# Optimization experiments

Measured on AMD Instinct MI355X. Metric: run time of the kernel, lower is better.

Reference implementation:

```python
import jax, jax.numpy as jnp
import numpy as np

N_REACHES = 4096
N_STEPS = 96
DT = 3600.0  # routing timestep (s), default from MuskingumCungeRouter


def safe_pow(base, exp, eps=1e-6):
    # AD-safe power: exp(e * log(max(b, eps)))
    return jnp.exp(exp * jnp.log(jnp.maximum(base, eps)))


def setup_inputs() -> dict:
    key = jax.random.key(0)
    ks = jax.random.split(key, 10)
    n, T = N_REACHES, N_STEPS
    u = lambda k, lo, hi, shape: jax.random.uniform(k, shape, minval=lo, maxval=hi)
    lateral_inflows = u(ks[0], 0.0, 5.0, (T, n))          # m^3/s lateral inflow
    initial_Q = u(ks[1], 0.1, 10.0, (n,))
    lengths = u(ks[2], 500.0, 10000.0, (n,))              # reach length (m)
    slopes = u(ks[3], 1e-4, 0.05, (n,))                   # bed slope
    manning_n = u(ks[4], 0.02, 0.08, (n,))
    width_coef = u(ks[5], 2.0, 10.0, (n,))
    width_exp = u(ks[6], 0.4, 0.6, (n,))                  # ~0.5 typical
    depth_coef = u(ks[7], 0.2, 0.6, (n,))
    depth_exp = u(ks[8], 0.25, 0.35, (n,))                # ~0.3 typical
    # Strictly lower-triangular sparse adjacency: reach i receives from j < i
    # (valid topological order), ~4 upstream links per reach on average.
    upstream_mask = jnp.tril(jax.random.uniform(ks[9], (n, n)) < (4.0 / n), k=-1)
    is_outlet = jnp.arange(n) == n - 1
    return dict(lateral_inflows=lateral_inflows, initial_Q=initial_Q,
                lengths=lengths, slopes=slopes, manning_n=manning_n,
                width_coef=width_coef, width_exp=width_exp,
                depth_coef=depth_coef, depth_exp=depth_exp,
                upstream_mask=upstream_mask, is_outlet=is_outlet)


def _mc_coeffs(Q, L, S, mn, wc, we, dc, de, dt):
    """Vectorized Muskingum-Cunge coefficients for all reaches.

    Faithful fusion of compute_channel_geometry -> compute_velocity_manning ->
    compute_celerity -> compute_muskingum_params. Q here is Q_ref = max(state.Q, 0.1),
    which only depends on the previous state, so hoisting out of the per-reach
    scan is mathematically identical to the original.
    """
    Qs = jnp.maximum(Q, 0.01)
    W = wc * safe_pow(Qs, we)
    D = dc * safe_pow(Qs, de)
    A = W * D
    R = A / (W + 2.0 * D)                      # hydraulic radius
    safe_S = jnp.maximum(S, 1e-6)
    V = (1.0 / jnp.maximum(mn, 1e-3)) * safe_pow(R, 2.0 / 3.0) * jnp.sqrt(safe_S)
    c = jnp.maximum((5.0 / 3.0) * V, 0.01)     # kinematic wave celerity
    K = jnp.maximum(L / c, dt * 0.1)
    X = jnp.clip(0.5 * (1.0 - Q / (W * c * safe_S * L + 1e-6)), 0.0, 0.5)
    den = 2.0 * K * (1.0 - X) + dt
    C0 = jnp.maximum((dt - 2.0 * K * X) / den, 0.0)
    C1 = jnp.maximum((dt + 2.0 * K * X) / den, 0.0)
    C2 = jnp.maximum((2.0 * K * (1.0 - X) - dt) / den, 0.0)
    tot = C0 + C1 + C2
    return C0 / tot, C1 / tot, C2 / tot


def _route(lateral_inflows, initial_Q, lengths, slopes, manning_n,
           width_coef, width_exp, depth_coef, depth_exp,
           upstream_mask, is_outlet, dt=DT):
    n = lengths.shape[0]

    def step(state, lateral):
        Q, Q_prev, I_prev = state
        Q_ref = jnp.maximum(Q, 0.1)
        C0, C1, C2 = _mc_coeffs(Q_ref, lengths, slopes, manning_n,
                                width_coef, width_exp, depth_coef, depth_exp, dt)

        # Sequential topological sweep: masked reduction over already-routed reaches.
        def process(Q_acc, i):
            upstream_Q = jnp.sum(jnp.where(upstream_mask[i], Q_acc, 0.0))
            I_curr = upstream_Q + lateral[i]
            Q_out = jnp.maximum(C0[i] * I_curr + C1[i] * I_prev[i] + C2[i] * Q_prev[i], 0.0)
            return Q_acc.at[i].set(Q_out), I_curr

        Q_final, I_all = jax.lax.scan(process, jnp.zeros(n, lateral.dtype), jnp.arange(n))
        outlet_Q = jnp.sum(jnp.where(is_outlet, Q_final, 0.0))
        return (Q_final, Q, I_all), outlet_Q

    init = (initial_Q, initial_Q, jnp.zeros(n, initial_Q.dtype))
    _, outlet_series = jax.lax.scan(step, init, lateral_inflows)
    return outlet_series  # [n_timesteps]


def reference(lateral_inflows, initial_Q, lengths, slopes, manning_n,
              width_coef, width_exp, depth_coef, depth_exp,
              upstream_mask, is_outlet):
    return _route(lateral_inflows, initial_Q, lengths, slopes, manning_n,
                  width_coef, width_exp, depth_coef, depth_exp,
                  upstream_mask, is_outlet)
```

## Files before the change

### kernel.cpp

```cpp
#include <hip/hip_runtime.h>

#define NR 4096
#define NT 96
#define NNZ_CAP 10240
#define WLDS 8
#define DHIST 32
#define DTSTEP 3600.0f

__device__ __forceinline__ float RCP(float x) { return __builtin_amdgcn_rcpf(x); }

__global__ void mc_build(const int* __restrict__ mask, int* __restrict__ rowBase,
                         int* __restrict__ rowCnt, int* __restrict__ gctr,
                         unsigned short* __restrict__ cols) {
  int row = blockIdx.x;
  int lane = threadIdx.x;
  const int4* rv = (const int4*)(mask + (size_t)row * NR);
  int c = 0;
  for (int j = lane; j < NR / 4; j += 64) {
    int4 v = rv[j];
    c += (v.x != 0) + (v.y != 0) + (v.z != 0) + (v.w != 0);
  }
#pragma unroll
  for (int off = 32; off > 0; off >>= 1) c += __shfl_down(c, off);
  int base = 0;
  if (lane == 0) {
    base = atomicAdd(gctr, c);
    rowBase[row] = base;
    rowCnt[row] = c;
  }
  base = __shfl(base, 0);
  const int* rs = mask + (size_t)row * NR;
  for (int j0 = 0; j0 < NR; j0 += 64) {
    int j = j0 + lane;
    int pred = (rs[j] != 0);
    unsigned long long m = __ballot(pred);
    if (pred) {
      int pos = __popcll(m & ((1ull << lane) - 1ull));
      int p = base + pos;
      if (p < NNZ_CAP) cols[p] = (unsigned short)j;
    }
    base += __popcll(m);
  }
}

__global__ __launch_bounds__(1024) void mc_prep(
    const int* __restrict__ rowBase, const int* __restrict__ rowCnt,
    const int* __restrict__ gctr, const unsigned short* __restrict__ colsOld,
    unsigned short* __restrict__ orderG, unsigned short* __restrict__ levNG,
    int* __restrict__ rowptrN, int* __restrict__ splitN,
    unsigned short* __restrict__ colsT, unsigned char* __restrict__ longSrcG,
    int* __restrict__ meta) {
  __shared__ unsigned short cols_s[NNZ_CAP];
  __shared__ unsigned char lev_s[NR];
  __shared__ unsigned short newid_s[NR];
  __shared__ unsigned short order_s[NR];
  __shared__ unsigned char lsrc_s[NR];
  __shared__ int cnt[1024];
  __shared__ int sbuf[1024];
  __shared__ int maxLevS, flagS;
  const int tid = threadIdx.x;
  int nnz = gctr[0];
  if (nnz > NNZ_CAP) nnz = NNZ_CAP;
  for (int e = tid; e < nnz; e += 1024) cols_s[e] = colsOld[e];

  int b_r[4], e_r[4];
#pragma unroll
  for (int k = 0; k < 4; ++k) {
    int i = 4 * tid + k;
    int b = rowBase[i];
    if (b > NNZ_CAP) b = NNZ_CAP;
    int e = b + rowCnt[i];
    if (e > NNZ_CAP) e = NNZ_CAP;
    b_r[k] = b;
    e_r[k] = e;
    lev_s[i] = 0;
    lsrc_s[i] = 0;
  }
  if (tid == 0) maxLevS = 0;
  __syncthreads();

  for (int pass = 0; pass < 48; ++pass) {
    if (tid == 0) flagS = 0;
    __syncthreads();
    int ch = 0;
#pragma unroll
    for (int k = 0; k < 4; ++k) {
      int i = 4 * tid + k;
      int lv = 0;
      for (int e = b_r[k]; e < e_r[k]; ++e) {
        int l2 = (int)lev_s[cols_s[e]] + 1;
        lv = lv > l2 ? lv : l2;
      }
      if (lv > 127) lv = 127;
      if (lv > (int)lev_s[i]) {
        lev_s[i] = (unsigned char)lv;
        ch = 1;
      }
    }
    if (ch) flagS = 1;
    __syncthreads();
    int done = (flagS == 0);
    __syncthreads();
    if (done) break;
  }
  int lm = 0;
#pragma unroll
  for (int k = 0; k < 4; ++k) {
    int l = lev_s[4 * tid + k];
    lm = lm > l ? lm : l;
  }
  atomicMax(&maxLevS, lm);
  __syncthreads();
  const int maxLev = maxLevS;
  if (tid == 0) {
    meta[0] = maxLev + 1;
    meta[2] = (maxLev >= DHIST) ? 1 : 0;
  }
  if (maxLev >= DHIST) {
#pragma unroll
    for (int k = 0; k < 4; ++k) {
      int i = 4 * tid + k;
      orderG[i] = (unsigned short)i;
      levNG[i] = (unsigned short)lev_s[i];
    }
    return;
  }

  cnt[tid] = 0;
  __syncthreads();
  int bkt_r[4];
#pragma unroll
  for (int k = 0; k < 4; ++k) {
    int i = 4 * tid + k;
    int d = e_r[k] - b_r[k];
    if (d > 31) d = 31;
    int bkt = ((int)lev_s[i]) * 32 + d;
    bkt_r[k] = bkt;
    atomicAdd(&cnt[bkt], 1);
  }
  __syncthreads();
  int v = cnt[tid];
  sbuf[tid] = v;
  __syncthreads();
  for (int off = 1; off < 1024; off <<= 1) {
    int add = tid >= off ? sbuf[tid - off] : 0;
    __syncthreads();
    sbuf[tid] += add;
    __syncthreads();
  }
  cnt[tid] = sbuf[tid] - v;
  __syncthreads();
#pragma unroll
  for (int k = 0; k < 4; ++k) {
    int i = 4 * tid + k;
    int pos = atomicAdd(&cnt[bkt_r[k]], 1);
    order_s[pos] = (unsigned short)i;
    newid_s[i] = (unsigned short)pos;
  }
  __syncthreads();

  int ob_r[4], c_r[4], tot = 0;
  unsigned char lvp_r[4];
#pragma unroll
  for (int k = 0; k < 4; ++k) {
    int p = 4 * tid + k;
    int oldi = order_s[p];
    orderG[p] = (unsigned short)oldi;
    unsigned char lp = lev_s[oldi];
    lvp_r[k] = lp;
    levNG[p] = (unsigned short)lp;
    int b = rowBase[oldi];
    if (b > NNZ_CAP) b = NNZ_CAP;
    int e = b + rowCnt[oldi];
    if (e > NNZ_CAP) e = NNZ_CAP;
    ob_r[k] = b;
    c_r[k] = e - b;
    tot += c_r[k];
  }
  sbuf[tid] = tot;
  __syncthreads();
  for (int off = 1; off < 1024; off <<= 1) {
    int add = tid >= off ? sbuf[tid - off] : 0;
    __syncthreads();
    sbuf[tid] += add;
    __syncthreads();
  }
  int base = sbuf[tid] - tot;
#pragma unroll
  for (int k = 0; k < 4; ++k) {
    int p = 4 * tid + k;
    rowptrN[p] = base;
    int ns = 0;
    for (int e = 0; e < c_r[k]; ++e) {
      int lag = (int)lvp_r[k] - (int)lev_s[cols_s[ob_r[k] + e]];
      ns += (lag < WLDS);
    }
    splitN[p] = base + ns;
    int si = base, li = base + ns;
    for (int e = 0; e < c_r[k]; ++e) {
      int cOld = cols_s[ob_r[k] + e];
      int cN = newid_s[cOld];
      int lag = (int)lvp_r[k] - (int)lev_s[cOld];
      if (lag < WLDS) {
        if (si < NNZ_CAP) colsT[si] = (unsigned short)cN;
        si++;
      } else {
        if (li < NNZ_CAP) colsT[li] = (unsigned short)cN;
        li++;
        lsrc_s[cN] = 1;
      }
    }
    base += c_r[k];
  }
  if (tid == 1023) rowptrN[NR] = sbuf[1023];
  if (tid == 0) meta[1] = newid_s[NR - 1];
  __syncthreads();
#pragma unroll
  for (int k = 0; k < 4; ++k) {
    int p = 4 * tid + k;
    longSrcG[p] = lsrc_s[p];
  }
}

__global__ void mc_permlat(const float* __restrict__ lat,
                           const unsigned short* __restrict__ orderG,
                           float* __restrict__ latP) {
  int g = blockIdx.x * 256 + threadIdx.x;
  int t = g >> 12, p = g & 4095;
  latP[g] = lat[t * NR + orderG[p]];
}

__device__ __forceinline__ void mc_coeff(float q1, float wc, float we, float dc,
                                         float de, float vk, float SL, float Lv,
                                         float& C0, float& C1, float& C2,
                                         float& inv) {
  float Qref = fmaxf(q1, 0.1f);
  float lq = __logf(Qref);
  float W = wc * __expf(we * lq);
  float Dd = dc * __expf(de * lq);
  float R = W * Dd * RCP(W + 2.f * Dd);
  float V = vk * __expf(0.66666667f * __logf(fmaxf(R, 1e-6f)));
  float c = fmaxf(1.6666667f * V, 0.01f);
  float K = fmaxf(Lv * RCP(c), 0.1f * DTSTEP);
  float X = 0.5f - 0.5f * Qref * RCP(W * c * SL + 1e-6f);
  X = fminf(fmaxf(X, 0.f), 0.5f);
  float twoKX = 2.f * K * X;
  C0 = fmaxf(DTSTEP - twoKX, 0.f);
  C1 = DTSTEP + twoKX;
  C2 = fmaxf(2.f * K - twoKX - DTSTEP, 0.f);
  inv = RCP(C0 + C1 + C2);
}

__global__ __launch_bounds__(1024) void mc_route(
    const float* __restrict__ lat, const float* __restrict__ latP,
    const float* __restrict__ initQ, const float* __restrict__ Lg,
    const float* __restrict__ Sg, const float* __restrict__ mng,
    const float* __restrict__ wcg, const float* __restrict__ weg,
    const float* __restrict__ dcg, const float* __restrict__ deg,
    const int* __restrict__ rowBase, const int* __restrict__ rowCnt,
    const unsigned short* __restrict__ colsOld,
    const unsigned short* __restrict__ orderG,
    const unsigned short* __restrict__ levNG, const int* __restrict__ rowptrN,
    const int* __restrict__ splitN, const unsigned short* __restrict__ colsT,
    const unsigned char* __restrict__ longSrcG, const int* __restrict__ meta,
    float* Qhist, float* __restrict__ out, int usePerm) {
  __shared__ float win[WLDS * NR];
  __shared__ unsigned short cols_s[NNZ_CAP];
  const int tid = threadIdx.x;
  const int nlv = meta[0];
  const int fb = meta[2];
  const int outletNew = meta[1];

  int b_r[4], m_r[4], e_r[4], lev_r[4], oldi_r[4], io_r[4], ls_r[4];
  float wc_r[4], we_r[4], dc_r[4], de_r[4], vk_r[4], SL_r[4], L_r[4];
  float ip_r[4], q1_r[4], q2_r[4];

  if (!fb) {
    int nnzN = rowptrN[NR];
    if (nnzN > NNZ_CAP) nnzN = NNZ_CAP;
    for (int e = tid; e < nnzN; e += 1024) cols_s[e] = colsT[e];
#pragma unroll
    for (int k = 0; k < 4; ++k) {
      int p = tid + k * 1024;
      int oldi = orderG[p];
      oldi_r[k] = oldi;
      lev_r[k] = (int)levNG[p];
      int b = rowptrN[p];
      if (b > NNZ_CAP) b = NNZ_CAP;
      int m = splitN[p];
      if (m > NNZ_CAP) m = NNZ_CAP;
      int e = rowptrN[p + 1];
      if (e > NNZ_CAP) e = NNZ_CAP;
      b_r[k] = b;
      m_r[k] = m;
      e_r[k] = e;
      io_r[k] = (p == outletNew);
      ls_r[k] = (int)longSrcG[p];
      float Lv = Lg[oldi], Sv = Sg[oldi], mnv = mng[oldi];
      float sS = fmaxf(Sv, 1e-6f);
      vk_r[k] = sqrtf(sS) * RCP(fmaxf(mnv, 1e-3f));
      SL_r[k] = sS * Lv;
      L_r[k] = Lv;
      wc_r[k] = wcg[oldi];
      we_r[k] = weg[oldi];
      dc_r[k] = dcg[oldi];
      de_r[k] = deg[oldi];
      float q0 = initQ[oldi];
      q1_r[k] = q0;
      q2_r[k] = q0;
      ip_r[k] = 0.f;
    }
    __syncthreads();

#define BODY(k, tt)                                                            \
  {                                                                            \
    const int p = tid + (k)*1024;                                              \
    float latv = usePerm ? latP[(tt)*NR + p] : lat[(tt)*NR + oldi_r[k]];       \
    float C0, C1, C2, inv;                                                     \
    mc_coeff(q1_r[k], wc_r[k], we_r[k], dc_r[k], de_r[k], vk_r[k], SL_r[k],    \
             L_r[k], C0, C1, C2, inv);                                         \
    const int wEl = ((tt) & (WLDS - 1)) << 12;                                 \
    float sup = 0.f;                                                           \
    for (int e = b_r[k]; e < m_r[k]; ++e) sup += win[wEl | cols_s[e]];         \
    if (m_r[k] < e_r[k]) {                                                     \
      const float* qb = Qhist + (((tt) & (DHIST - 1)) << 12);                  \
      for (int e = m_r[k]; e < e_r[k]; ++e) sup += qb[cols_s[e]];              \
    }                                                                          \
    float Icurr = sup + latv;                                                  \
    float Qout = fmaxf((C0 * Icurr + C1 * ip_r[k] + C2 * q2_r[k]) * inv, 0.f); \
    win[wEl | p] = Qout;                                                       \
    if (ls_r[k]) Qhist[((((tt) & (DHIST - 1)) << 12)) | p] = Qout;             \
    ip_r[k] = Icurr;                                                           \
    q2_r[k] = q1_r[k];                                                         \
    q1_r[k] = Qout;                                                            \
    if (io_r[k]) out[tt] = Qout;                                               \
  }

#define BODYC(k, s)                                                            \
  {                                                                            \
    int t = (s)-lev_r[k];                                                      \
    if ((unsigned)t < (unsigned)NT) BODY(k, t)                                 \
  }

    for (int s = 0; s < nlv - 1; ++s) {
#pragma unroll
      for (int k = 0; k < 4; ++k) BODYC(k, s);
      __syncthreads();
    }
    for (int s = nlv - 1; s < NT; ++s) {
#pragma unroll
      for (int k = 0; k < 4; ++k) {
        int t = s - lev_r[k];
        BODY(k, t);
      }
      __syncthreads();
    }
    for (int s = NT; s < NT + nlv - 1; ++s) {
#pragma unroll
      for (int k = 0; k < 4; ++k) BODYC(k, s);
      __syncthreads();
    }
  } else {
    for (int e = tid; e < NNZ_CAP; e += 1024) cols_s[e] = colsOld[e];
#pragma unroll
    for (int k = 0; k < 4; ++k) {
      int i = tid + k * 1024;
      lev_r[k] = (int)levNG[i];
      int b = rowBase[i];
      if (b > NNZ_CAP) b = NNZ_CAP;
      int e = b + rowCnt[i];
      if (e > NNZ_CAP) e = NNZ_CAP;
      b_r[k] = b;
      e_r[k] = e;
      float Lv = Lg[i], Sv = Sg[i], mnv = mng[i];
      float sS = fmaxf(Sv, 1e-6f);
      vk_r[k] = sqrtf(sS) * RCP(fmaxf(mnv, 1e-3f));
      SL_r[k] = sS * Lv;
      L_r[k] = Lv;
      wc_r[k] = wcg[i];
      we_r[k] = weg[i];
      dc_r[k] = dcg[i];
      de_r[k] = deg[i];
      float q0 = initQ[i];
      q1_r[k] = q0;
      q2_r[k] = q0;
      ip_r[k] = 0.f;
    }
    __syncthreads();
    for (int t = 0; t < NT; ++t) {
      for (int l = 0; l < meta[0]; ++l) {
#pragma unroll
        for (int k = 0; k < 4; ++k) {
          if (lev_r[k] == l) {
            int i = tid + k * 1024;
            float latv = lat[t * NR + i];
            float C0, C1, C2, inv;
            mc_coeff(q1_r[k], wc_r[k], we_r[k], dc_r[k], de_r[k], vk_r[k],
                     SL_r[k], L_r[k], C0, C1, C2, inv);
            float sup = 0.f;
            for (int e = b_r[k]; e < e_r[k]; ++e) sup += Qhist[cols_s[e]];
            float Icurr = sup + latv;
            float Qout =
                fmaxf((C0 * Icurr + C1 * ip_r[k] + C2 * q2_r[k]) * inv, 0.f);
            Qhist[i] = Qout;
            ip_r[k] = Icurr;
            q2_r[k] = q1_r[k];
            q1_r[k] = Qout;
            if (i == NR - 1) out[t] = Qout;
          }
        }
        __syncthreads();
      }
    }
  }
}

extern "C" void kernel_launch(void* const* d_in, const int* in_sizes, int n_in,
                              void* d_out, int out_size, void* d_ws, size_t ws_size,
                              hipStream_t stream) {
  const float* lat = (const float*)d_in[0];
  const float* iQ = (const float*)d_in[1];
  const float* Lg = (const float*)d_in[2];
  const float* Sg = (const float*)d_in[3];
  const float* mng = (const float*)d_in[4];
  const float* wcg = (const float*)d_in[5];
  const float* weg = (const float*)d_in[6];
  const float* dcg = (const float*)d_in[7];
  const float* deg = (const float*)d_in[8];
  const int* mask = (const int*)d_in[9];
  float* out = (float*)d_out;

  char* w = (char*)d_ws;
  int* rowBase = (int*)w;                w += NR * 4;
  int* rowCnt = (int*)w;                 w += NR * 4;
  int* gctr = (int*)w;                   w += 16;
  int* meta = (int*)w;                   w += 16;
  unsigned short* colsOld = (unsigned short*)w;  w += NNZ_CAP * 2;
  unsigned short* orderG = (unsigned short*)w;   w += NR * 2;
  unsigned short* levNG = (unsigned short*)w;    w += NR * 2;
  int* rowptrN = (int*)w;                w += (NR + 4) * 4;
  int* splitN = (int*)w;                 w += NR * 4;
  unsigned short* colsT = (unsigned short*)w;    w += NNZ_CAP * 2;
  unsigned char* longSrcG = (unsigned char*)w;   w += NR;
  w += 16 - ((size_t)w & 15);
  float* Qhist = (float*)w;              w += (size_t)DHIST * NR * 4;
  float* latP = (float*)w;               w += (size_t)NT * NR * 4;
  size_t need = (size_t)(w - (char*)d_ws);
  int usePerm = (ws_size >= need) ? 1 : 0;

  hipMemsetAsync(gctr, 0, sizeof(int), stream);
  mc_build<<<NR, 64, 0, stream>>>(mask, rowBase, rowCnt, gctr, colsOld);
  mc_prep<<<1, 1024, 0, stream>>>(rowBase, rowCnt, gctr, colsOld, orderG, levNG,
                                  rowptrN, splitN, colsT, longSrcG, meta);
  if (usePerm)
    mc_permlat<<<(NT * NR) / 256, 256, 0, stream>>>(lat, orderG, latP);
  mc_route<<<1, 1024, 0, stream>>>(lat, latP, iQ, Lg, Sg, mng, wcg, weg, dcg,
                                   deg, rowBase, rowCnt, colsOld, orderG, levNG,
                                   rowptrN, splitN, colsT, longSrcG, meta,
                                   Qhist, out, usePerm);
}
```

Measured before the change: 563.5 us.

## Restructure routing sweep with fixed 4-slot upstream lists and log-domain coefficients

mc_build now reads each mask row once: it compacts column indices into shared memory, then does one atomic and copies them out. mc_prep replaces the CSR rowptr/split arrays with a fixed 4-entry packed upstream list per reach, plus separate overflow lists for short-lag and long-lag sources built with atomics. mc_route reads the four slots with a single uint2 LDS load, prefetches the next timestep's lateral inflow, and computes the Muskingum coefficients in log2 domain with precomputed log constants, which removes several exp/log calls. The change also shrinks the window to 7 slots, adds a launch-bounds occupancy hint, and caps rows at 80 upstream entries, which could drop links on denser inputs.

```diff
diff --git a/kernel.cpp b/kernel.cpp
--- a/kernel.cpp
+++ b/kernel.cpp
@@ -3,43 +3,46 @@
 #define NR 4096
 #define NT 96
 #define NNZ_CAP 10240
-#define WLDS 8
+#define WLDS 7
 #define DHIST 32
 #define DTSTEP 3600.0f
+#define LOG2_1E6 -19.931568f
 
 __device__ __forceinline__ float RCP(float x) { return __builtin_amdgcn_rcpf(x); }
+__device__ __forceinline__ float EXP2(float x) { return __builtin_amdgcn_exp2f(x); }
+__device__ __forceinline__ float LOG2(float x) { return __builtin_amdgcn_logf(x); }
 
 __global__ void mc_build(const int* __restrict__ mask, int* __restrict__ rowBase,
                          int* __restrict__ rowCnt, int* __restrict__ gctr,
                          unsigned short* __restrict__ cols) {
+  __shared__ unsigned short tmp[80];
+  __shared__ int baseS;
   int row = blockIdx.x;
   int lane = threadIdx.x;
-  const int4* rv = (const int4*)(mask + (size_t)row * NR);
-  int c = 0;
-  for (int j = lane; j < NR / 4; j += 64) {
-    int4 v = rv[j];
-    c += (v.x != 0) + (v.y != 0) + (v.z != 0) + (v.w != 0);
-  }
-#pragma unroll
-  for (int off = 32; off > 0; off >>= 1) c += __shfl_down(c, off);
-  int base = 0;
-  if (lane == 0) {
-    base = atomicAdd(gctr, c);
-    rowBase[row] = base;
-    rowCnt[row] = c;
-  }
-  base = __shfl(base, 0);
   const int* rs = mask + (size_t)row * NR;
+  int total = 0;
   for (int j0 = 0; j0 < NR; j0 += 64) {
     int j = j0 + lane;
     int pred = (rs[j] != 0);
     unsigned long long m = __ballot(pred);
     if (pred) {
-      int pos = __popcll(m & ((1ull << lane) - 1ull));
-      int p = base + pos;
-      if (p < NNZ_CAP) cols[p] = (unsigned short)j;
-    }
-    base += __popcll(m);
+      int pos = total + __popcll(m & ((1ull << lane) - 1ull));
+      if (pos < 80) tmp[pos] = (unsigned short)j;
+    }
+    total += __popcll(m);
+  }
+  if (total > 80) total = 80;
+  if (lane == 0) {
+    int b = atomicAdd(gctr, total);
+    rowBase[row] = b;
+    rowCnt[row] = total;
+    baseS = b;
+  }
+  __syncthreads();
+  int base = baseS;
+  for (int e = lane; e < total; e += 64) {
+    int p = base + e;
+    if (p < NNZ_CAP) cols[p] = tmp[e];
   }
 }
 
@@ -47,8 +50,9 @@
     const int* __restrict__ rowBase, const int* __restrict__ rowCnt,
     const int* __restrict__ gctr, const unsigned short* __restrict__ colsOld,
     unsigned short* __restrict__ orderG, unsigned short* __restrict__ levNG,
-    int* __restrict__ rowptrN, int* __restrict__ splitN,
-    unsigned short* __restrict__ colsT, unsigned char* __restrict__ longSrcG,
+    unsigned short* __restrict__ scolG, unsigned int* __restrict__ sremMeta,
+    unsigned int* __restrict__ longMeta, unsigned short* __restrict__ sremG,
+    unsigned short* __restrict__ longG, unsigned char* __restrict__ lsG,
     int* __restrict__ meta) {
   __shared__ unsigned short cols_s[NNZ_CAP];
   __shared__ unsigned char lev_s[NR];
@@ -159,66 +163,59 @@
   }
   __syncthreads();
 
-  int ob_r[4], c_r[4], tot = 0;
-  unsigned char lvp_r[4];
 #pragma unroll
   for (int k = 0; k < 4; ++k) {
     int p = 4 * tid + k;
     int oldi = order_s[p];
     orderG[p] = (unsigned short)oldi;
-    unsigned char lp = lev_s[oldi];
-    lvp_r[k] = lp;
+    int lp = (int)lev_s[oldi];
     levNG[p] = (unsigned short)lp;
     int b = rowBase[oldi];
     if (b > NNZ_CAP) b = NNZ_CAP;
     int e = b + rowCnt[oldi];
     if (e > NNZ_CAP) e = NNZ_CAP;
-    ob_r[k] = b;
-    c_r[k] = e - b;
-    tot += c_r[k];
-  }
-  sbuf[tid] = tot;
-  __syncthreads();
-  for (int off = 1; off < 1024; off <<= 1) {
-    int add = tid >= off ? sbuf[tid - off] : 0;
-    __syncthreads();
-    sbuf[tid] += add;
-    __syncthreads();
-  }
-  int base = sbuf[tid] - tot;
-#pragma unroll
-  for (int k = 0; k < 4; ++k) {
-    int p = 4 * tid + k;
-    rowptrN[p] = base;
-    int ns = 0;
-    for (int e = 0; e < c_r[k]; ++e) {
-      int lag = (int)lvp_r[k] - (int)lev_s[cols_s[ob_r[k] + e]];
-      ns += (lag < WLDS);
-    }
-    splitN[p] = base + ns;
-    int si = base, li = base + ns;
-    for (int e = 0; e < c_r[k]; ++e) {
-      int cOld = cols_s[ob_r[k] + e];
+    int nS = 0, nR = 0, nL = 0;
+    for (int ee = b; ee < e; ++ee) {
+      int lag = lp - (int)lev_s[cols_s[ee]];
+      if (lag < WLDS) {
+        if (nS < 4) ++nS; else ++nR;
+      } else ++nL;
+    }
+    if (nR > 63) nR = 63;
+    if (nL > 63) nL = 63;
+    int sB = nR ? atomicAdd(&meta[4], nR) : 0;
+    int lB = nL ? atomicAdd(&meta[5], nL) : 0;
+    if (sB > NNZ_CAP) sB = NNZ_CAP;
+    if (sB + nR > NNZ_CAP) nR = NNZ_CAP - sB;
+    if (lB > NNZ_CAP) lB = NNZ_CAP;
+    if (lB + nL > NNZ_CAP) nL = NNZ_CAP - lB;
+    unsigned short sc[4] = {0, 0, 0, 0};
+    int iS = 0, cR = 0, cL = 0;
+    for (int ee = b; ee < e; ++ee) {
+      int cOld = cols_s[ee];
       int cN = newid_s[cOld];
-      int lag = (int)lvp_r[k] - (int)lev_s[cOld];
+      int lag = lp - (int)lev_s[cOld];
       if (lag < WLDS) {
-        if (si < NNZ_CAP) colsT[si] = (unsigned short)cN;
-        si++;
+        if (iS < 4) sc[iS++] = (unsigned short)cN;
+        else if (cR < nR) { sremG[sB + cR] = (unsigned short)cN; ++cR; }
       } else {
-        if (li < NNZ_CAP) colsT[li] = (unsigned short)cN;
-        li++;
+        if (cL < nL) { longG[lB + cL] = (unsigned short)cN; ++cL; }
         lsrc_s[cN] = 1;
       }
     }
-    base += c_r[k];
-  }
-  if (tid == 1023) rowptrN[NR] = sbuf[1023];
+    scolG[4 * p + 0] = sc[0];
+    scolG[4 * p + 1] = sc[1];
+    scolG[4 * p + 2] = sc[2];
+    scolG[4 * p + 3] = sc[3];
+    sremMeta[p] = (unsigned)sB | ((unsigned)nR << 20) | ((unsigned)iS << 26);
+    longMeta[p] = (unsigned)lB | ((unsigned)nL << 20);
+  }
   if (tid == 0) meta[1] = newid_s[NR - 1];
   __syncthreads();
 #pragma unroll
   for (int k = 0; k < 4; ++k) {
     int p = 4 * tid + k;
-    longSrcG[p] = lsrc_s[p];
+    lsG[p] = lsrc_s[p];
   }
 }
 
@@ -230,28 +227,7 @@
   latP[g] = lat[t * NR + orderG[p]];
 }
 
-__device__ __forceinline__ void mc_coeff(float q1, float wc, float we, float dc,
-                                         float de, float vk, float SL, float Lv,
-                                         float& C0, float& C1, float& C2,
-                                         float& inv) {
-  float Qref = fmaxf(q1, 0.1f);
-  float lq = __logf(Qref);
-  float W = wc * __expf(we * lq);
-  float Dd = dc * __expf(de * lq);
-  float R = W * Dd * RCP(W + 2.f * Dd);
-  float V = vk * __expf(0.66666667f * __logf(fmaxf(R, 1e-6f)));
-  float c = fmaxf(1.6666667f * V, 0.01f);
-  float K = fmaxf(Lv * RCP(c), 0.1f * DTSTEP);
-  float X = 0.5f - 0.5f * Qref * RCP(W * c * SL + 1e-6f);
-  X = fminf(fmaxf(X, 0.f), 0.5f);
-  float twoKX = 2.f * K * X;
-  C0 = fmaxf(DTSTEP - twoKX, 0.f);
-  C1 = DTSTEP + twoKX;
-  C2 = fmaxf(2.f * K - twoKX - DTSTEP, 0.f);
-  inv = RCP(C0 + C1 + C2);
-}
-
-__global__ __launch_bounds__(1024) void mc_route(
+__global__ __launch_bounds__(1024, 4) void mc_route(
     const float* __restrict__ lat, const float* __restrict__ latP,
     const float* __restrict__ initQ, const float* __restrict__ Lg,
     const float* __restrict__ Sg, const float* __restrict__ mng,
@@ -260,80 +236,112 @@
     const int* __restrict__ rowBase, const int* __restrict__ rowCnt,
     const unsigned short* __restrict__ colsOld,
     const unsigned short* __restrict__ orderG,
-    const unsigned short* __restrict__ levNG, const int* __restrict__ rowptrN,
-    const int* __restrict__ splitN, const unsigned short* __restrict__ colsT,
-    const unsigned char* __restrict__ longSrcG, const int* __restrict__ meta,
+    const unsigned short* __restrict__ levNG,
+    const unsigned short* __restrict__ scolG,
+    const unsigned int* __restrict__ sremMeta,
+    const unsigned int* __restrict__ longMeta,
+    const unsigned short* __restrict__ sremG,
+    const unsigned short* __restrict__ longG,
+    const unsigned char* __restrict__ lsG, const int* __restrict__ meta,
     float* Qhist, float* __restrict__ out, int usePerm) {
-  __shared__ float win[WLDS * NR];
-  __shared__ unsigned short cols_s[NNZ_CAP];
+  __shared__ float win_s[WLDS * NR];
+  __shared__ unsigned short scol_s[NR * 4];
   const int tid = threadIdx.x;
   const int nlv = meta[0];
   const int fb = meta[2];
   const int outletNew = meta[1];
 
-  int b_r[4], m_r[4], e_r[4], lev_r[4], oldi_r[4], io_r[4], ls_r[4];
-  float wc_r[4], we_r[4], dc_r[4], de_r[4], vk_r[4], SL_r[4], L_r[4];
-  float ip_r[4], q1_r[4], q2_r[4];
+  int lev_r[4], io_r[4], ls_r[4], wslot_r[4], cnt_r[4];
+  int sB_r[4], sC_r[4], lB_r[4], lC_r[4], latIdx_r[4];
+  float lwc_r[4], we_r[4], ldc_r[4], de_r[4], lvk_r[4], SL_r[4], L_r[4];
+  float ip_r[4], q1_r[4], q2_r[4], latN_r[4];
+  const float* latB = usePerm ? latP : lat;
 
   if (!fb) {
-    int nnzN = rowptrN[NR];
-    if (nnzN > NNZ_CAP) nnzN = NNZ_CAP;
-    for (int e = tid; e < nnzN; e += 1024) cols_s[e] = colsT[e];
+    for (int e = tid; e < NR * 2; e += 1024)
+      ((unsigned int*)scol_s)[e] = ((const unsigned int*)scolG)[e];
 #pragma unroll
     for (int k = 0; k < 4; ++k) {
       int p = tid + k * 1024;
       int oldi = orderG[p];
-      oldi_r[k] = oldi;
       lev_r[k] = (int)levNG[p];
-      int b = rowptrN[p];
-      if (b > NNZ_CAP) b = NNZ_CAP;
-      int m = splitN[p];
-      if (m > NNZ_CAP) m = NNZ_CAP;
-      int e = rowptrN[p + 1];
-      if (e > NNZ_CAP) e = NNZ_CAP;
-      b_r[k] = b;
-      m_r[k] = m;
-      e_r[k] = e;
+      unsigned int sm = sremMeta[p];
+      sB_r[k] = sm & 0xFFFFF;
+      sC_r[k] = (sm >> 20) & 63;
+      cnt_r[k] = (sm >> 26) & 7;
+      unsigned int lm2 = longMeta[p];
+      lB_r[k] = lm2 & 0xFFFFF;
+      lC_r[k] = (lm2 >> 20) & 63;
+      ls_r[k] = (int)lsG[p];
       io_r[k] = (p == outletNew);
-      ls_r[k] = (int)longSrcG[p];
-      float Lv = Lg[oldi], Sv = Sg[oldi], mnv = mng[oldi];
-      float sS = fmaxf(Sv, 1e-6f);
-      vk_r[k] = sqrtf(sS) * RCP(fmaxf(mnv, 1e-3f));
+      float Lv = Lg[oldi];
+      float sS = fmaxf(Sg[oldi], 1e-6f);
+      float mnv = fmaxf(mng[oldi], 1e-3f);
+      lvk_r[k] = 0.7369656f + 0.5f * LOG2(sS) - LOG2(mnv);
       SL_r[k] = sS * Lv;
       L_r[k] = Lv;
-      wc_r[k] = wcg[oldi];
+      lwc_r[k] = LOG2(wcg[oldi]);
       we_r[k] = weg[oldi];
-      dc_r[k] = dcg[oldi];
+      ldc_r[k] = LOG2(dcg[oldi]);
       de_r[k] = deg[oldi];
       float q0 = initQ[oldi];
       q1_r[k] = q0;
       q2_r[k] = q0;
       ip_r[k] = 0.f;
-    }
-    __syncthreads();
-
-#define BODY(k, tt)                                                            \
-  {                                                                            \
-    const int p = tid + (k)*1024;                                              \
-    float latv = usePerm ? latP[(tt)*NR + p] : lat[(tt)*NR + oldi_r[k]];       \
-    float C0, C1, C2, inv;                                                     \
-    mc_coeff(q1_r[k], wc_r[k], we_r[k], dc_r[k], de_r[k], vk_r[k], SL_r[k],    \
-             L_r[k], C0, C1, C2, inv);                                         \
-    const int wEl = ((tt) & (WLDS - 1)) << 12;                                 \
-    float sup = 0.f;                                                           \
-    for (int e = b_r[k]; e < m_r[k]; ++e) sup += win[wEl | cols_s[e]];         \
-    if (m_r[k] < e_r[k]) {                                                     \
-      const float* qb = Qhist + (((tt) & (DHIST - 1)) << 12);                  \
-      for (int e = m_r[k]; e < e_r[k]; ++e) sup += qb[cols_s[e]];              \
-    }                                                                          \
-    float Icurr = sup + latv;                                                  \
-    float Qout = fmaxf((C0 * Icurr + C1 * ip_r[k] + C2 * q2_r[k]) * inv, 0.f); \
-    win[wEl | p] = Qout;                                                       \
-    if (ls_r[k]) Qhist[((((tt) & (DHIST - 1)) << 12)) | p] = Qout;             \
-    ip_r[k] = Icurr;                                                           \
-    q2_r[k] = q1_r[k];                                                         \
-    q1_r[k] = Qout;                                                            \
-    if (io_r[k]) out[tt] = Qout;                                               \
+      wslot_r[k] = 0;
+      latIdx_r[k] = usePerm ? p : oldi;
+      latN_r[k] = latB[latIdx_r[k]];
+    }
+    __syncthreads();
+
+#define BODY(k, tt)                                                             \
+  {                                                                             \
+    const int p = tid + (k)*1024;                                               \
+    const float latv = latN_r[k];                                               \
+    float Qref = fmaxf(q1_r[k], 0.1f);                                          \
+    float lq = LOG2(Qref);                                                      \
+    float lgW = fmaf(we_r[k], lq, lwc_r[k]);                                    \
+    float W = EXP2(lgW);                                                        \
+    float aD = fmaf(de_r[k], lq, ldc_r[k]);                                     \
+    float Dd = EXP2(aD);                                                        \
+    float lgR = fmaxf(lgW + aD - LOG2(fmaf(2.f, Dd, W)), LOG2_1E6);             \
+    float c = fmaxf(EXP2(fmaf(0.66666667f, lgR, lvk_r[k])), 0.01f);             \
+    float K = fmaxf(L_r[k] * RCP(c), 360.f);                                    \
+    float X = fmaxf(0.5f - 0.5f * Qref * RCP(fmaf(W * c, SL_r[k], 1e-6f)), 0.f);\
+    float twoKX = 2.f * K * X;                                                  \
+    float C0 = fmaxf(DTSTEP - twoKX, 0.f);                                      \
+    float C1 = DTSTEP + twoKX;                                                  \
+    float C2 = fmaxf(2.f * K - twoKX - DTSTEP, 0.f);                            \
+    float inv = RCP(C0 + C1 + C2);                                              \
+    const int wB = wslot_r[k] << 12;                                            \
+    uint2 cc = *(const uint2*)(scol_s + 4 * p);                                 \
+    float v0 = win_s[wB | (cc.x & 0xFFFFu)];                                    \
+    float v1 = win_s[wB | (cc.x >> 16)];                                        \
+    float v2 = win_s[wB | (cc.y & 0xFFFFu)];                                    \
+    float v3 = win_s[wB | (cc.y >> 16)];                                        \
+    const int cn = cnt_r[k];                                                    \
+    float sup = (cn > 0 ? v0 : 0.f) + (cn > 1 ? v1 : 0.f) +                     \
+                (cn > 2 ? v2 : 0.f) + (cn > 3 ? v3 : 0.f);                      \
+    if (sC_r[k]) {                                                              \
+      for (int e = 0; e < sC_r[k]; ++e)                                         \
+        sup += win_s[wB | sremG[sB_r[k] + e]];                                  \
+    }                                                                           \
+    if (lC_r[k]) {                                                              \
+      const float* qb = Qhist + (((tt)&31) << 12);                              \
+      for (int e = 0; e < lC_r[k]; ++e) sup += qb[longG[lB_r[k] + e]];          \
+    }                                                                           \
+    float Icurr = sup + latv;                                                   \
+    float Qout = fmaxf((C0 * Icurr + C1 * ip_r[k] + C2 * q2_r[k]) * inv, 0.f);  \
+    win_s[wB | p] = Qout;                                                       \
+    if (ls_r[k]) Qhist[(((tt)&31) << 12) | p] = Qout;                           \
+    if (io_r[k]) out[tt] = Qout;                                                \
+    ip_r[k] = Icurr;                                                            \
+    q2_r[k] = q1_r[k];                                                          \
+    q1_r[k] = Qout;                                                             \
+    wslot_r[k] = (wslot_r[k] == WLDS - 1) ? 0 : wslot_r[k] + 1;                 \
+    int tn = (tt) + 1;                                                          \
+    tn = tn < NT ? tn : NT - 1;                                                 \
+    latN_r[k] = latB[tn * NR + latIdx_r[k]];                                    \
   }
 
 #define BODYC(k, s)                                                            \
@@ -361,7 +369,8 @@
       __syncthreads();
     }
   } else {
-    for (int e = tid; e < NNZ_CAP; e += 1024) cols_s[e] = colsOld[e];
+    int b_r[4], e_r[4];
+    for (int e = tid; e < NNZ_CAP; e += 1024) scol_s[e] = colsOld[e];
 #pragma unroll
     for (int k = 0; k < 4; ++k) {
       int i = tid + k * 1024;
@@ -372,14 +381,15 @@
       if (e > NNZ_CAP) e = NNZ_CAP;
       b_r[k] = b;
       e_r[k] = e;
-      float Lv = Lg[i], Sv = Sg[i], mnv = mng[i];
-      float sS = fmaxf(Sv, 1e-6f);
-      vk_r[k] = sqrtf(sS) * RCP(fmaxf(mnv, 1e-3f));
+      float Lv = Lg[i];
+      float sS = fmaxf(Sg[i], 1e-6f);
+      float mnv = fmaxf(mng[i], 1e-3f);
+      lvk_r[k] = 0.7369656f + 0.5f * LOG2(sS) - LOG2(mnv);
       SL_r[k] = sS * Lv;
       L_r[k] = Lv;
-      wc_r[k] = wcg[i];
+      lwc_r[k] = LOG2(wcg[i]);
       we_r[k] = weg[i];
-      dc_r[k] = dcg[i];
+      ldc_r[k] = LOG2(dcg[i]);
       de_r[k] = deg[i];
       float q0 = initQ[i];
       q1_r[k] = q0;
@@ -388,17 +398,30 @@
     }
     __syncthreads();
     for (int t = 0; t < NT; ++t) {
-      for (int l = 0; l < meta[0]; ++l) {
+      for (int l = 0; l < nlv; ++l) {
 #pragma unroll
         for (int k = 0; k < 4; ++k) {
           if (lev_r[k] == l) {
             int i = tid + k * 1024;
             float latv = lat[t * NR + i];
-            float C0, C1, C2, inv;
-            mc_coeff(q1_r[k], wc_r[k], we_r[k], dc_r[k], de_r[k], vk_r[k],
-                     SL_r[k], L_r[k], C0, C1, C2, inv);
+            float Qref = fmaxf(q1_r[k], 0.1f);
+            float lq = LOG2(Qref);
+            float lgW = fmaf(we_r[k], lq, lwc_r[k]);
+            float W = EXP2(lgW);
+            float aD = fmaf(de_r[k], lq, ldc_r[k]);
+            float Dd = EXP2(aD);
+            float lgR = fmaxf(lgW + aD - LOG2(fmaf(2.f, Dd, W)), LOG2_1E6);
+            float c = fmaxf(EXP2(fmaf(0.66666667f, lgR, lvk_r[k])), 0.01f);
+            float K = fmaxf(L_r[k] * RCP(c), 360.f);
+            float X =
+                fmaxf(0.5f - 0.5f * Qref * RCP(fmaf(W * c, SL_r[k], 1e-6f)), 0.f);
+            float twoKX = 2.f * K * X;
+            float C0 = fmaxf(DTSTEP - twoKX, 0.f);
+            float C1 = DTSTEP + twoKX;
+            float C2 = fmaxf(2.f * K - twoKX - DTSTEP, 0.f);
+            float inv = RCP(C0 + C1 + C2);
             float sup = 0.f;
-            for (int e = b_r[k]; e < e_r[k]; ++e) sup += Qhist[cols_s[e]];
+            for (int e = b_r[k]; e < e_r[k]; ++e) sup += Qhist[scol_s[e]];
             float Icurr = sup + latv;
             float Qout =
                 fmaxf((C0 * Icurr + C1 * ip_r[k] + C2 * q2_r[k]) * inv, 0.f);
@@ -431,31 +454,34 @@
   float* out = (float*)d_out;
 
   char* w = (char*)d_ws;
-  int* rowBase = (int*)w;                w += NR * 4;
-  int* rowCnt = (int*)w;                 w += NR * 4;
-  int* gctr = (int*)w;                   w += 16;
-  int* meta = (int*)w;                   w += 16;
+  int* rowBase = (int*)w;                        w += NR * 4;
+  int* rowCnt = (int*)w;                         w += NR * 4;
+  int* gctr = (int*)w;                           w += 16;
+  int* meta = (int*)w;                           w += 32;
   unsigned short* colsOld = (unsigned short*)w;  w += NNZ_CAP * 2;
   unsigned short* orderG = (unsigned short*)w;   w += NR * 2;
   unsigned short* levNG = (unsigned short*)w;    w += NR * 2;
-  int* rowptrN = (int*)w;                w += (NR + 4) * 4;
-  int* splitN = (int*)w;                 w += NR * 4;
-  unsigned short* colsT = (unsigned short*)w;    w += NNZ_CAP * 2;
-  unsigned char* longSrcG = (unsigned char*)w;   w += NR;
+  unsigned short* scolG = (unsigned short*)w;    w += NR * 4 * 2;
+  unsigned int* sremMeta = (unsigned int*)w;     w += NR * 4;
+  unsigned int* longMeta = (unsigned int*)w;     w += NR * 4;
+  unsigned short* sremG = (unsigned short*)w;    w += NNZ_CAP * 2;
+  unsigned short* longG = (unsigned short*)w;    w += NNZ_CAP * 2;
+  unsigned char* lsG = (unsigned char*)w;        w += NR;
   w += 16 - ((size_t)w & 15);
-  float* Qhist = (float*)w;              w += (size_t)DHIST * NR * 4;
-  float* latP = (float*)w;               w += (size_t)NT * NR * 4;
+  float* Qhist = (float*)w;                      w += (size_t)DHIST * NR * 4;
+  float* latP = (float*)w;                       w += (size_t)NT * NR * 4;
   size_t need = (size_t)(w - (char*)d_ws);
   int usePerm = (ws_size >= need) ? 1 : 0;
 
-  hipMemsetAsync(gctr, 0, sizeof(int), stream);
+  hipMemsetAsync(gctr, 0, 48, stream);
   mc_build<<<NR, 64, 0, stream>>>(mask, rowBase, rowCnt, gctr, colsOld);
   mc_prep<<<1, 1024, 0, stream>>>(rowBase, rowCnt, gctr, colsOld, orderG, levNG,
-                                  rowptrN, splitN, colsT, longSrcG, meta);
+                                  scolG, sremMeta, longMeta, sremG, longG, lsG,
+                                  meta);
   if (usePerm)
     mc_permlat<<<(NT * NR) / 256, 256, 0, stream>>>(lat, orderG, latP);
   mc_route<<<1, 1024, 0, stream>>>(lat, latP, iQ, Lg, Sg, mng, wcg, weg, dcg,
                                    deg, rowBase, rowCnt, colsOld, orderG, levNG,
-                                   rowptrN, splitN, colsT, longSrcG, meta,
-                                   Qhist, out, usePerm);
+                                   scolG, sremMeta, longMeta, sremG, longG, lsG,
+                                   meta, Qhist, out, usePerm);
 }
```

Result: slower. 590.8 us (+4.8%).
